# Kernel optimization log

Hardware: AMD Instinct MI355X
Metric: run time of the kernel (lower is better)

## Reference

```python
import jax, jax.numpy as jnp
import numpy as np

T, N_SAT, G_SAT, HID, IN = 256, 1024, 2048, 256, 32

def _make_sids(key):
    # per-timestep unique visible-satellite ids (matches dict-keyed state, no dup scatter)
    keys = jax.random.split(key, T)
    return jax.vmap(lambda k: jax.random.permutation(k, G_SAT)[:N_SAT])(keys).astype(jnp.int32)

def setup_inputs() -> dict:
    key = jax.random.key(0)
    ks = jax.random.split(key, 16)
    s = 0.05
    return {
        "x_rec": jax.random.normal(ks[0], (T, 1, IN), jnp.float32),
        "x_sat": jax.random.normal(ks[1], (T, N_SAT, IN), jnp.float32),
        "y_true": jax.random.normal(ks[2], (1, 2), jnp.float32),
        "W_rec": jax.random.normal(ks[3], (4, IN, HID), jnp.float32) * s,
        "b_rec": jax.random.normal(ks[4], (4, HID), jnp.float32) * s,
        "W_sat": jax.random.normal(ks[5], (4, IN, HID), jnp.float32) * s,
        "b_sat": jax.random.normal(ks[6], (4, HID), jnp.float32) * s,
        "s2r_lw": jax.random.normal(ks[7], (4, HID, HID), jnp.float32) * s,
        "s2r_lb": jax.random.normal(ks[8], (4, HID), jnp.float32) * s,
        "s2r_rw": jax.random.normal(ks[9], (4, HID, HID), jnp.float32) * s,
        "r2s_lw": jax.random.normal(ks[10], (4, HID, HID), jnp.float32) * s,
        "r2s_lb": jax.random.normal(ks[11], (4, HID), jnp.float32) * s,
        "r2s_rw": jax.random.normal(ks[12], (4, HID, HID), jnp.float32) * s,
        "W_out": jax.random.normal(ks[13], (HID, 2), jnp.float32) * s,
        "b_out": jax.random.normal(ks[14], (2,), jnp.float32) * s,
        "s_ids": _make_sids(ks[15]),
    }

def _gates(pre):
    # pre: [4, ..., HID] in gate order (i, f, c, o)
    return (jax.nn.sigmoid(pre[0]), jax.nn.sigmoid(pre[1]),
            jnp.tanh(pre[2]), jax.nn.sigmoid(pre[3]))

def reference(x_rec, x_sat, y_true, W_rec, b_rec, W_sat, b_sat,
              s2r_lw, s2r_lb, s2r_rw, r2s_lw, r2s_lb, r2s_rw,
              W_out, b_out, s_ids):
    hid = W_out.shape[0]

    def step(carry, inp):
        h_rec, c_rec, Hg, Cg = carry          # h_rec/c_rec: [hid]; Hg/Cg: [G, hid]
        xr, xs, sid = inp                      # xr: [1, in]; xs: [N, in]; sid: [N]
        h_sat = Hg[sid]                        # gather visible satellite states [N, hid]
        c_sat = Cg[sid]
        # per-gate input projections
        xr_p = jnp.einsum('i,gio->go', xr[0], W_rec) + b_rec          # [4, hid]
        xs_p = jnp.einsum('ni,gio->gno', xs, W_sat) + b_sat[:, None]  # [4, N, hid]
        # SAGEConv sat->rec: mean over all visible sats (star topology)
        mean_sat = jnp.mean(h_sat, axis=0)                            # [hid]
        conv_rec = (jnp.einsum('h,gho->go', mean_sat, s2r_lw) + s2r_lb
                    + jnp.einsum('h,gho->go', h_rec, s2r_rw))         # [4, hid]
        # SAGEConv rec->sat: each sat's sole neighbor is the receiver
        conv_sat = ((jnp.einsum('h,gho->go', h_rec, r2s_lw) + r2s_lb)[:, None, :]
                    + jnp.einsum('nh,gho->gno', h_sat, r2s_rw))       # [4, N, hid]
        i_r, f_r, t_r, o_r = _gates(xr_p + conv_rec)
        c_rec_n = f_r * c_rec + i_r * t_r
        h_rec_n = o_r * jnp.tanh(c_rec_n)
        i_s, f_s, t_s, o_s = _gates(xs_p + conv_sat)
        c_sat_n = f_s * c_sat + i_s * t_s
        h_sat_n = o_s * jnp.tanh(c_sat_n)
        Hg = Hg.at[sid].set(h_sat_n)
        Cg = Cg.at[sid].set(c_sat_n)
        return (h_rec_n, c_rec_n, Hg, Cg), None

    init = (jnp.zeros((hid,), x_rec.dtype), jnp.zeros((hid,), x_rec.dtype),
            jnp.zeros((G_SAT, hid), x_rec.dtype), jnp.zeros((G_SAT, hid), x_rec.dtype))
    (h_rec, _, _, _), _ = jax.lax.scan(step, init, (x_rec, x_sat, s_ids))
    pred = h_rec[None, :] @ W_out + b_out   # dropout is identity in eval mode
    return pred, y_true
```

## Files before the change

### kernel.cpp

```cpp
#include <hip/hip_runtime.h>
#include <cstddef>

#define T_STEPS  256
#define NSAT     1024
#define GSAT     2048
#define HID      256
#define IN_DIM   32
#define KTOT     544

typedef short  s16x8 __attribute__((ext_vector_type(8)));
typedef short  s16x4 __attribute__((ext_vector_type(4)));
typedef float  f32x4 __attribute__((ext_vector_type(4)));
typedef unsigned short ushort_t;

__device__ inline ushort_t f2bf(float f) {
    unsigned u = __builtin_bit_cast(unsigned, f);
    u += 0x7fffu + ((u >> 16) & 1u);
    return (ushort_t)(u >> 16);
}
__device__ inline float bf2f(ushort_t h) {
    unsigned u = ((unsigned)h) << 16;
    return __builtin_bit_cast(float, u);
}
__device__ inline float sigm(float x) { return 1.f / (1.f + __expf(-x)); }
__device__ inline float tanh_(float x) {
    float a = fabsf(x);
    float e = __expf(-2.f * a);
    float r = (1.f - e) / (1.f + e);
    return copysignf(r, x);
}

__global__ void k_zero(float* p, size_t n) {
    size_t i = (size_t)blockIdx.x * blockDim.x + threadIdx.x;
    size_t stride = (size_t)gridDim.x * blockDim.x;
    for (; i < n; i += stride) p[i] = 0.f;
}

__global__ void k_bconv(const float* __restrict__ r2s_rw,
                        const float* __restrict__ W_sat,
                        const float* __restrict__ r2s_lw,
                        ushort_t* __restrict__ BsatT) {
    int c = blockIdx.x;
    int g = (c >> 3) & 3, o = (c >> 5) * 8 + (c & 7);
    for (int k = threadIdx.x; k < KTOT; k += 256) {
        float v;
        if (k < 256)      v = r2s_rw[((size_t)g * 256 + k) * 256 + o];
        else if (k < 288) v = W_sat[((size_t)g * 32 + (k - 256)) * 256 + o];
        else              v = r2s_lw[((size_t)g * 256 + (k - 288)) * 256 + o];
        BsatT[(size_t)c * KTOT + k] = f2bf(v);
    }
}

__global__ void k_biasC(const float* __restrict__ r2s_lb, const float* __restrict__ b_sat,
                        float* __restrict__ biasC) {
    int c = blockIdx.x * 256 + threadIdx.x;
    if (c < 1024) {
        int g = (c >> 3) & 3, o = (c >> 5) * 8 + (c & 7);
        biasC[c] = r2s_lb[g * 256 + o] + b_sat[g * 256 + o];
    }
}

__global__ void k_inv(const int* __restrict__ s_ids, ushort_t* __restrict__ pos_inv) {
    int t = blockIdx.x;
    for (int n = threadIdx.x; n < NSAT; n += 256)
        pos_inv[(size_t)t * GSAT + s_ids[(size_t)t * NSAT + n]] = (ushort_t)(n + 1);
}

__global__ void k_asrc(const int* __restrict__ s_ids, const ushort_t* __restrict__ pos_inv,
                       int* __restrict__ asrc) {
    int t = blockIdx.x;
    for (int n = threadIdx.x; n < NSAT; n += 256) {
        int j = s_ids[(size_t)t * NSAT + n];
        int e = 1024 + j;
        if (t > 0) {
            int p = (int)pos_inv[(size_t)(t - 1) * GSAT + j] - 1;
            if (p >= 0) e = p;
        }
        asrc[(size_t)t * NSAT + n] = e;
    }
}

__global__ void k_bits(const int* __restrict__ s_ids, const ushort_t* __restrict__ pos_inv,
                       unsigned* __restrict__ nxt_bits) {
    int t = blockIdx.x, w = threadIdx.x;
    unsigned bits = 0;
    if (t + 1 < T_STEPS) {
        for (int i = 0; i < 32; i++) {
            int j = s_ids[(size_t)t * NSAT + w * 32 + i];
            if (pos_inv[(size_t)(t + 1) * GSAT + j] > 0) bits |= (1u << i);
        }
    }
    nxt_bits[t * 32 + w] = bits;
}

__global__ void k_old(const int* __restrict__ s_ids, const ushort_t* __restrict__ pos_inv,
                      short* __restrict__ old_src, int* __restrict__ old_cnt) {
    int t = blockIdx.x;
    if (t + 1 >= T_STEPS) return;
    for (int n = threadIdx.x; n < NSAT; n += 256) {
        int j = s_ids[(size_t)(t + 1) * NSAT + n];
        if (pos_inv[(size_t)t * GSAT + j] == 0) {
            int slot = atomicAdd(&old_cnt[t], 1);
            short e = (short)(-(j + 1));
            if (t > 0) {
                int p = (int)pos_inv[(size_t)(t - 1) * GSAT + j] - 1;
                if (p >= 0) e = (short)p;
            }
            old_src[(size_t)t * NSAT + slot] = e;
        }
    }
}

__global__ void k_wtb(const float* __restrict__ in, ushort_t* __restrict__ outT) {
    __shared__ float tl[32][33];
    int g = blockIdx.z;
    int h0 = blockIdx.x * 32, o0 = blockIdx.y * 32;
    int lx = threadIdx.x & 31, ly = threadIdx.x >> 5;
#pragma unroll
    for (int i = 0; i < 32; i += 8)
        tl[ly + i][lx] = in[((size_t)g * 256 + h0 + ly + i) * 256 + o0 + lx];
    __syncthreads();
#pragma unroll
    for (int i = 0; i < 32; i += 8)
        outT[((size_t)g * 256 + o0 + ly + i) * 256 + h0 + lx] = f2bf(tl[lx][ly + i]);
}

__global__ void k_wrt(const float* __restrict__ W_rec, float* __restrict__ W_recT) {
    int idx = blockIdx.x * 256 + threadIdx.x;
    int g = idx >> 8, o = idx & 255;
#pragma unroll
    for (int i = 0; i < 32; i++)
        W_recT[(size_t)idx * 32 + i] = W_rec[((size_t)g * 32 + i) * 256 + o];
}

__launch_bounds__(256)
__global__ void k_step(int t,
    const float* __restrict__ x_rec, const float* __restrict__ x_sat,
    const float* __restrict__ b_rec, const float* __restrict__ s2r_lb,
    const int* __restrict__ s_ids, const int* __restrict__ asrc,
    const unsigned* __restrict__ nxt_bits,
    const short* __restrict__ old_src, const int* __restrict__ old_cnt,
    const ushort_t* __restrict__ BsatT, const float* __restrict__ biasC,
    const ushort_t* __restrict__ s2r_rwT, const ushort_t* __restrict__ s2r_lwT,
    const float* __restrict__ W_recT,
    float* __restrict__ meanN,
    float* __restrict__ oldpart,
    float* __restrict__ crec,
    float* __restrict__ pre_rec,
    ushort_t* __restrict__ Hg_bf, float* __restrict__ Cg,
    const ushort_t* __restrict__ HnP, ushort_t* __restrict__ HnC,
    const float* __restrict__ CnP, float* __restrict__ CnC)
{
    const int b = blockIdx.x, tid = threadIdx.x;
    const float* preP  = pre_rec + ((t + 1) & 1) * 1024;
    const float* crecP = crec + (t & 1) * 256;

    if (b < 256) {
        const int by = b >> 5, bxc = b & 31;
        __shared__ ushort_t hr_bfs[256];
        __shared__ float    bias_s[32];
        __shared__ float    pre_s[128][33];

        const int w = tid >> 6, l = tid & 63;
        const int lr = l & 15, kb = (l >> 4) * 8;
        const int r0 = w * 32 + lr, r1 = r0 + 16;
        const int* asrc_t = asrc + (size_t)t * NSAT + by * 128;

        const int e0 = asrc_t[r0], e1 = asrc_t[r1];
        if (tid < 32) bias_s[tid] = biasC[bxc * 32 + tid];
        const int n_ep = tid >> 1, oi0_ep = (tid & 1) * 4;
        const int og0_ep = bxc * 8 + oi0_ep;
        const int en_ep = asrc_t[n_ep];
        const float* csrc = (en_ep < 1024) ? CnP + (size_t)en_ep * HID + og0_ep
                                           : Cg + (size_t)(en_ep - 1024) * HID + og0_ep;
        f32x4 cold = *(const f32x4*)csrc;
        ushort_t shv[4]; float scv[4]; int sjp[4];
        if (t > 0) {
#pragma unroll
            for (int i = 0; i < 4; i++) {
                int n = b * 4 + i;
                sjp[i] = s_ids[(size_t)(t - 1) * NSAT + n];
                shv[i] = HnP[(size_t)n * HID + tid];
                scv[i] = CnP[(size_t)n * HID + tid];
            }
        }
        {
            float h = 0.f;
            if (t > 0) {
                float pi = preP[tid], pf = preP[256 + tid], pc = preP[512 + tid], po = preP[768 + tid];
                float cp = (t >= 2) ? crecP[tid] : 0.f;
                float cn = sigm(pf) * cp + sigm(pi) * tanh_(pc);
                h = sigm(po) * tanh_(cn);
            }
            hr_bfs[tid] = f2bf(h);
        }

        const ushort_t* a0 = (e0 < 1024) ? HnP + (size_t)e0 * HID : Hg_bf + (size_t)(e0 - 1024) * HID;
        const ushort_t* a1 = (e1 < 1024) ? HnP + (size_t)e1 * HID : Hg_bf + (size_t)(e1 - 1024) * HID;
        const ushort_t* bp0 = BsatT + ((size_t)(bxc * 32 + lr)) * KTOT;
        const ushort_t* bp1 = bp0 + (size_t)16 * KTOT;
        f32x4 a00 = {0.f,0.f,0.f,0.f}, a01 = a00, a10 = a00, a11 = a00;
#pragma unroll
        for (int kc = 0; kc < 8; kc++) {
            int k0 = kc * 32 + kb;
            s16x8 af0 = *(const s16x8*)(a0 + k0);
            s16x8 af1 = *(const s16x8*)(a1 + k0);
            s16x8 bv0 = *(const s16x8*)(bp0 + k0);
            s16x8 bv1 = *(const s16x8*)(bp1 + k0);
            a00 = __builtin_amdgcn_mfma_f32_16x16x32_bf16(af0, bv0, a00, 0, 0, 0);
            a01 = __builtin_amdgcn_mfma_f32_16x16x32_bf16(af0, bv1, a01, 0, 0, 0);
            a10 = __builtin_amdgcn_mfma_f32_16x16x32_bf16(af1, bv0, a10, 0, 0, 0);
            a11 = __builtin_amdgcn_mfma_f32_16x16x32_bf16(af1, bv1, a11, 0, 0, 0);
        }
        {
            const float* ax0 = x_sat + ((size_t)t * NSAT + by * 128 + r0) * IN_DIM + kb;
            const float* ax1 = x_sat + ((size_t)t * NSAT + by * 128 + r1) * IN_DIM + kb;
            f32x4 x00 = *(const f32x4*)ax0, x01 = *(const f32x4*)(ax0 + 4);
            f32x4 x10 = *(const f32x4*)ax1, x11 = *(const f32x4*)(ax1 + 4);
            s16x8 af0, af1;
#pragma unroll
            for (int e = 0; e < 4; e++) {
                af0[e] = (short)f2bf(x00[e]); af0[4 + e] = (short)f2bf(x01[e]);
                af1[e] = (short)f2bf(x10[e]); af1[4 + e] = (short)f2bf(x11[e]);
            }
            int k0 = 256 + kb;
            s16x8 bv0 = *(const s16x8*)(bp0 + k0);
            s16x8 bv1 = *(const s16x8*)(bp1 + k0);
            a00 = __builtin_amdgcn_mfma_f32_16x16x32_bf16(af0, bv0, a00, 0, 0, 0);
            a01 = __builtin_amdgcn_mfma_f32_16x16x32_bf16(af0, bv1, a01, 0, 0, 0);
            a10 = __builtin_amdgcn_mfma_f32_16x16x32_bf16(af1, bv0, a10, 0, 0, 0);
            a11 = __builtin_amdgcn_mfma_f32_16x16x32_bf16(af1, bv1, a11, 0, 0, 0);
        }
        __syncthreads();
#pragma unroll
        for (int kc = 0; kc < 8; kc++) {
            int k0 = 288 + kc * 32 + kb;
            s16x8 af = *(const s16x8*)(hr_bfs + (k0 - 288));
            s16x8 bv0 = *(const s16x8*)(bp0 + k0);
            s16x8 bv1 = *(const s16x8*)(bp1 + k0);
            a00 = __builtin_amdgcn_mfma_f32_16x16x32_bf16(af, bv0, a00, 0, 0, 0);
            a01 = __builtin_amdgcn_mfma_f32_16x16x32_bf16(af, bv1, a01, 0, 0, 0);
            a10 = __builtin_amdgcn_mfma_f32_16x16x32_bf16(af, bv0, a10, 0, 0, 0);
            a11 = __builtin_amdgcn_mfma_f32_16x16x32_bf16(af, bv1, a11, 0, 0, 0);
        }
#pragma unroll
        for (int rr = 0; rr < 4; rr++) {
            int ro = (l >> 4) * 4 + rr;
            pre_s[w * 32 + ro][lr]           = a00[rr];
            pre_s[w * 32 + ro][16 + lr]      = a01[rr];
            pre_s[w * 32 + 16 + ro][lr]      = a10[rr];
            pre_s[w * 32 + 16 + ro][16 + lr] = a11[rr];
        }
        __syncthreads();

        {
            int n = n_ep, oi0 = oi0_ep, og0 = og0_ep;
            int gr = by * 128 + n;
            bool nxt = (t + 1 < T_STEPS) && ((nxt_bits[t * 32 + (gr >> 5)] >> (gr & 31)) & 1u);
            f32x4 cnew, hf; s16x4 hnew;
#pragma unroll
            for (int e = 0; e < 4; e++) {
                int oi = oi0 + e;
                float pi = pre_s[n][oi]      + bias_s[oi];
                float pf = pre_s[n][8 + oi]  + bias_s[8 + oi];
                float pc = pre_s[n][16 + oi] + bias_s[16 + oi];
                float po = pre_s[n][24 + oi] + bias_s[24 + oi];
                float ig = sigm(pi), fg = sigm(pf), tg = tanh_(pc), oo = sigm(po);
                float cn = fg * cold[e] + ig * tg;
                float hn = oo * tanh_(cn);
                cnew[e] = cn; hf[e] = hn;
                hnew[e] = (short)f2bf(hn);
            }
            *(f32x4*)(CnC + (size_t)gr * HID + og0) = cnew;
            *(s16x4*)(HnC + (size_t)gr * HID + og0) = hnew;
#pragma unroll
            for (int e = 0; e < 4; e++) pre_s[n][oi0 + e] = nxt ? hf[e] : 0.f;
        }
        __syncthreads();
        if (t + 1 < T_STEPS && tid < 8) {
            float s = 0.f;
            for (int n = 0; n < 128; n++) s += pre_s[n][tid];
            meanN[((t + 1) & 1) * 2048 + by * 256 + bxc * 8 + tid] = s;
        }

        if (t > 0) {
#pragma unroll
            for (int i = 0; i < 4; i++) {
                Hg_bf[(size_t)sjp[i] * HID + tid] = shv[i];
                Cg[(size_t)sjp[i] * HID + tid]    = scv[i];
            }
        }
    } else {
        const int r = b - 256;
        __shared__ float mean_s[256], hr_s[256], xr_s[32];
        const int m_old = (t + 1 < T_STEPS) ? old_cnt[t] : 0;
        {
            float s = 0.f;
            const float* mp = meanN + (t & 1) * 2048;
#pragma unroll
            for (int p = 0; p < 8; p++) s += mp[p * 256 + tid];
            const float* op = oldpart + (t & 1) * 8192;
#pragma unroll 8
            for (int p = 0; p < 32; p++) s += op[p * 256 + tid];
            mean_s[tid] = s * (1.f / 1024.f);
        }
        {
            float h = 0.f, cn = 0.f;
            if (t > 0) {
                float pi = preP[tid], pf = preP[256 + tid], pc = preP[512 + tid], po = preP[768 + tid];
                float cp = (t >= 2) ? crecP[tid] : 0.f;
                cn = sigm(pf) * cp + sigm(pi) * tanh_(pc);
                h = sigm(po) * tanh_(cn);
            }
            hr_s[tid] = h;
            if (r == 0 && t > 0) crec[((t + 1) & 1) * 256 + tid] = cn;
        }
        if (tid < 32) xr_s[tid] = x_rec[(size_t)t * IN_DIM + tid];
        __syncthreads();
        float s_old = 0.f;
        {
            const short* osp = old_src + (size_t)t * NSAT;
#pragma unroll 2
            for (int k = r; k < m_old; k += 32) {
                int e = osp[k];
                const ushort_t* hp = (e >= 0) ? HnP + (size_t)e * HID
                                              : Hg_bf + (size_t)(-(e + 1)) * HID;
                s_old += bf2f(hp[tid]);
            }
        }
        {
            const int combo = tid >> 3, sub = tid & 7;
            const int g = combo >> 3, oo = combo & 7;
            const int o = r * 8 + oo;
            const ushort_t* rwp = s2r_rwT + ((size_t)(g * 256 + o)) * 256 + sub * 32;
            const ushort_t* lwp = s2r_lwT + ((size_t)(g * 256 + o)) * 256 + sub * 32;
            float part = 0.f;
#pragma unroll
            for (int q = 0; q < 4; q++) {
                s16x8 a = *(const s16x8*)(rwp + q * 8);
                s16x8 c = *(const s16x8*)(lwp + q * 8);
#pragma unroll
                for (int e = 0; e < 8; e++) {
                    int h = sub * 32 + q * 8 + e;
                    part += hr_s[h] * bf2f((ushort_t)a[e]) + mean_s[h] * bf2f((ushort_t)c[e]);
                }
            }
            {
                f32x4 wx = *(const f32x4*)(W_recT + ((size_t)(g * 256 + o)) * 32 + sub * 4);
#pragma unroll
                for (int e = 0; e < 4; e++) part += xr_s[sub * 4 + e] * wx[e];
            }
            part += __shfl_down(part, 4);
            part += __shfl_down(part, 2);
            part += __shfl_down(part, 1);
            if (sub == 0)
                pre_rec[(t & 1) * 1024 + g * 256 + o] =
                    part + b_rec[g * HID + o] + s2r_lb[g * HID + o];
        }
        if (t + 1 < T_STEPS)
            oldpart[((t + 1) & 1) * 8192 + r * 256 + tid] = s_old;
    }
}

__global__ void k_final(const float* __restrict__ pre_rec,
                        const float* __restrict__ crec,
                        const float* __restrict__ W_out,
                        const float* __restrict__ b_out,
                        const float* __restrict__ y_true,
                        float* __restrict__ out) {
    __shared__ float red[256];
    int o = threadIdx.x;
    const float* pre = pre_rec + ((T_STEPS - 1) & 1) * 1024;
    float pi = pre[o], pf = pre[256 + o], pc = pre[512 + o], po = pre[768 + o];
    float cp = crec[(T_STEPS & 1) * 256 + o];
    float cn = sigm(pf) * cp + sigm(pi) * tanh_(pc);
    float h = sigm(po) * tanh_(cn);
    for (int j = 0; j < 2; j++) {
        red[o] = h * W_out[o * 2 + j];
        __syncthreads();
        for (int s = 128; s > 0; s >>= 1) {
            if (o < s) red[o] += red[o + s];
            __syncthreads();
        }
        if (o == 0) out[j] = red[0] + b_out[j];
        __syncthreads();
    }
    if (o < 2) out[2 + o] = y_true[o];
}

extern "C" void kernel_launch(void* const* d_in, const int* in_sizes, int n_in,
                              void* d_out, int out_size, void* d_ws, size_t ws_size,
                              hipStream_t stream) {
    (void)in_sizes; (void)n_in; (void)out_size; (void)ws_size;
    const float* x_rec  = (const float*)d_in[0];
    const float* x_sat  = (const float*)d_in[1];
    const float* y_true = (const float*)d_in[2];
    const float* W_rec  = (const float*)d_in[3];
    const float* b_rec  = (const float*)d_in[4];
    const float* W_sat  = (const float*)d_in[5];
    const float* b_sat  = (const float*)d_in[6];
    const float* s2r_lw = (const float*)d_in[7];
    const float* s2r_lb = (const float*)d_in[8];
    const float* s2r_rw = (const float*)d_in[9];
    const float* r2s_lw = (const float*)d_in[10];
    const float* r2s_lb = (const float*)d_in[11];
    const float* r2s_rw = (const float*)d_in[12];
    const float* W_out  = (const float*)d_in[13];
    const float* b_out  = (const float*)d_in[14];
    const int*   s_ids  = (const int*)d_in[15];

    float* ws = (float*)d_ws;
    size_t off = 0;
    float*    meanN    = ws + off;              off += 4096;
    float*    oldpart  = ws + off;              off += 16384;
    float*    crec     = ws + off;              off += 512;
    float*    pre_rec  = ws + off;              off += 2048;
    int*      old_cnt  = (int*)(ws + off);      off += 256;
    ushort_t* Hg_bf    = (ushort_t*)(ws + off); off += 262144;
    float*    Cg       = ws + off;              off += 524288;
    ushort_t* pos_inv  = (ushort_t*)(ws + off); off += 262144;
    int*      asrc     = (int*)(ws + off);      off += 262144;
    unsigned* nxt_bits = (unsigned*)(ws + off); off += 8192;
    short*    old_src  = (short*)(ws + off);    off += 131072;
    ushort_t* HnewA    = (ushort_t*)(ws + off); off += 131072;
    ushort_t* HnewB    = (ushort_t*)(ws + off); off += 131072;
    float*    CnewA    = ws + off;              off += 262144;
    float*    CnewB    = ws + off;              off += 262144;
    ushort_t* BsatT    = (ushort_t*)(ws + off); off += 278528;
    float*    biasC    = ws + off;              off += 1024;
    ushort_t* s2r_rwT  = (ushort_t*)(ws + off); off += 131072;
    ushort_t* s2r_lwT  = (ushort_t*)(ws + off); off += 131072;
    float*    W_recT   = ws + off;              off += 32768;

    const size_t zcount = 4096 + 16384 + 512 + 2048 + 256 + 262144 + 524288 + 262144;
    hipLaunchKernelGGL(k_zero, dim3(2048), dim3(256), 0, stream, ws, zcount);
    hipLaunchKernelGGL(k_inv, dim3(T_STEPS), dim3(256), 0, stream, s_ids, pos_inv);
    hipLaunchKernelGGL(k_asrc, dim3(T_STEPS), dim3(256), 0, stream, s_ids, pos_inv, asrc);
    hipLaunchKernelGGL(k_bits, dim3(T_STEPS), dim3(32), 0, stream, s_ids, pos_inv, nxt_bits);
    hipLaunchKernelGGL(k_old, dim3(T_STEPS), dim3(256), 0, stream, s_ids, pos_inv, old_src, old_cnt);
    hipLaunchKernelGGL(k_bconv, dim3(1024), dim3(256), 0, stream, r2s_rw, W_sat, r2s_lw, BsatT);
    hipLaunchKernelGGL(k_biasC, dim3(4), dim3(256), 0, stream, r2s_lb, b_sat, biasC);
    hipLaunchKernelGGL(k_wtb, dim3(8, 8, 4), dim3(256), 0, stream, s2r_rw, s2r_rwT);
    hipLaunchKernelGGL(k_wtb, dim3(8, 8, 4), dim3(256), 0, stream, s2r_lw, s2r_lwT);
    hipLaunchKernelGGL(k_wrt, dim3(4), dim3(256), 0, stream, W_rec, W_recT);

    for (int t = 0; t < T_STEPS; t++) {
        const ushort_t* HnP = (t & 1) ? HnewA : HnewB;
        ushort_t*       HnC = (t & 1) ? HnewB : HnewA;
        const float*    CnP = (t & 1) ? CnewA : CnewB;
        float*          CnC = (t & 1) ? CnewB : CnewA;
        hipLaunchKernelGGL(k_step, dim3(288), dim3(256), 0, stream,
                           t, x_rec, x_sat, b_rec, s2r_lb,
                           s_ids, asrc, nxt_bits, old_src, old_cnt,
                           BsatT, biasC,
                           s2r_rwT, s2r_lwT, W_recT,
                           meanN, oldpart, crec, pre_rec,
                           Hg_bf, Cg, HnP, HnC, CnP, CnC);
    }
    hipLaunchKernelGGL(k_final, dim3(1), dim3(256), 0, stream,
                       pre_rec, crec, W_out, b_out, y_true, (float*)d_out);
}
```

Before: 3.604 ms.

## Hoist receiver r2s term out of MFMA, store cell state in bf16, write back only leavers

The receiver-to-satellite left-weight product is the same for every satellite row, so it is taken out of the per-row MFMA K loop (K shrinks from 544 to 288). Each block now computes it once as a small dot product into shared memory and adds it like a bias. Satellite cell state (global and ping-pong buffers) moves from fp32 to bf16, halving its traffic. Writebacks to the global state now cover only satellites that leave visibility, using a precomputed leaver list, instead of all previous-step rows. Storing the cell state in bf16 adds rounding error that builds up along the recurrence.

```diff
diff --git a/kernel.cpp b/kernel.cpp
--- a/kernel.cpp
+++ b/kernel.cpp
@@ -6,7 +6,7 @@
 #define GSAT     2048
 #define HID      256
 #define IN_DIM   32
-#define KTOT     544
+#define KTOT     288
 
 typedef short  s16x8 __attribute__((ext_vector_type(8)));
 typedef short  s16x4 __attribute__((ext_vector_type(4)));
@@ -38,17 +38,21 @@
 
 __global__ void k_bconv(const float* __restrict__ r2s_rw,
                         const float* __restrict__ W_sat,
-                        const float* __restrict__ r2s_lw,
                         ushort_t* __restrict__ BsatT) {
     int c = blockIdx.x;
     int g = (c >> 3) & 3, o = (c >> 5) * 8 + (c & 7);
     for (int k = threadIdx.x; k < KTOT; k += 256) {
-        float v;
-        if (k < 256)      v = r2s_rw[((size_t)g * 256 + k) * 256 + o];
-        else if (k < 288) v = W_sat[((size_t)g * 32 + (k - 256)) * 256 + o];
-        else              v = r2s_lw[((size_t)g * 256 + (k - 288)) * 256 + o];
+        float v = (k < 256) ? r2s_rw[((size_t)g * 256 + k) * 256 + o]
+                            : W_sat[((size_t)g * 32 + (k - 256)) * 256 + o];
         BsatT[(size_t)c * KTOT + k] = f2bf(v);
     }
+}
+
+__global__ void k_rlw(const float* __restrict__ r2s_lw, ushort_t* __restrict__ rlw_bf) {
+    int c = blockIdx.x;
+    int g = (c >> 3) & 3, o = (c >> 5) * 8 + (c & 7);
+    int h = threadIdx.x;
+    rlw_bf[(size_t)c * 256 + h] = f2bf(r2s_lw[((size_t)g * 256 + h) * 256 + o]);
 }
 
 __global__ void k_biasC(const float* __restrict__ r2s_lb, const float* __restrict__ b_sat,
@@ -111,6 +115,19 @@
     }
 }
 
+__global__ void k_lv(const int* __restrict__ s_ids, const ushort_t* __restrict__ pos_inv,
+                     int* __restrict__ lv, int* __restrict__ lv_cnt) {
+    int t = blockIdx.x;
+    if (t == 0) return;
+    for (int n = threadIdx.x; n < NSAT; n += 256) {
+        int j = s_ids[(size_t)(t - 1) * NSAT + n];
+        if (pos_inv[(size_t)t * GSAT + j] == 0) {
+            int slot = atomicAdd(&lv_cnt[t], 1);
+            lv[(size_t)t * NSAT + slot] = (n << 16) | j;
+        }
+    }
+}
+
 __global__ void k_wtb(const float* __restrict__ in, ushort_t* __restrict__ outT) {
     __shared__ float tl[32][33];
     int g = blockIdx.z;
@@ -137,19 +154,20 @@
 __global__ void k_step(int t,
     const float* __restrict__ x_rec, const float* __restrict__ x_sat,
     const float* __restrict__ b_rec, const float* __restrict__ s2r_lb,
-    const int* __restrict__ s_ids, const int* __restrict__ asrc,
-    const unsigned* __restrict__ nxt_bits,
+    const int* __restrict__ asrc, const unsigned* __restrict__ nxt_bits,
     const short* __restrict__ old_src, const int* __restrict__ old_cnt,
-    const ushort_t* __restrict__ BsatT, const float* __restrict__ biasC,
+    const int* __restrict__ lv, const int* __restrict__ lv_cnt,
+    const ushort_t* __restrict__ BsatT, const ushort_t* __restrict__ rlw_bf,
+    const float* __restrict__ biasC,
     const ushort_t* __restrict__ s2r_rwT, const ushort_t* __restrict__ s2r_lwT,
     const float* __restrict__ W_recT,
     float* __restrict__ meanN,
     float* __restrict__ oldpart,
     float* __restrict__ crec,
     float* __restrict__ pre_rec,
-    ushort_t* __restrict__ Hg_bf, float* __restrict__ Cg,
+    ushort_t* __restrict__ Hg_bf, ushort_t* __restrict__ Cg_bf,
     const ushort_t* __restrict__ HnP, ushort_t* __restrict__ HnC,
-    const float* __restrict__ CnP, float* __restrict__ CnC)
+    const ushort_t* __restrict__ CnP, ushort_t* __restrict__ CnC)
 {
     const int b = blockIdx.x, tid = threadIdx.x;
     const float* preP  = pre_rec + ((t + 1) & 1) * 1024;
@@ -159,6 +177,7 @@
         const int by = b >> 5, bxc = b & 31;
         __shared__ ushort_t hr_bfs[256];
         __shared__ float    bias_s[32];
+        __shared__ float    rl_s[32];
         __shared__ float    pre_s[128][33];
 
         const int w = tid >> 6, l = tid & 63;
@@ -171,18 +190,20 @@
         const int n_ep = tid >> 1, oi0_ep = (tid & 1) * 4;
         const int og0_ep = bxc * 8 + oi0_ep;
         const int en_ep = asrc_t[n_ep];
-        const float* csrc = (en_ep < 1024) ? CnP + (size_t)en_ep * HID + og0_ep
-                                           : Cg + (size_t)(en_ep - 1024) * HID + og0_ep;
-        f32x4 cold = *(const f32x4*)csrc;
-        ushort_t shv[4]; float scv[4]; int sjp[4];
-        if (t > 0) {
-#pragma unroll
-            for (int i = 0; i < 4; i++) {
-                int n = b * 4 + i;
-                sjp[i] = s_ids[(size_t)(t - 1) * NSAT + n];
-                shv[i] = HnP[(size_t)n * HID + tid];
-                scv[i] = CnP[(size_t)n * HID + tid];
-            }
+        const ushort_t* csrc = (en_ep < 1024) ? CnP + (size_t)en_ep * HID + og0_ep
+                                              : Cg_bf + (size_t)(en_ep - 1024) * HID + og0_ep;
+        s16x4 cold4 = *(const s16x4*)csrc;
+        const int lv_m = lv_cnt[t];
+        ushort_t pH[4], pC[4]; int pJ[4];
+#pragma unroll
+        for (int i = 0; i < 4; i++) {
+            int k = b + i * 256;
+            if (k < lv_m) {
+                int pv = lv[(size_t)t * NSAT + k];
+                int pos = pv >> 16; pJ[i] = pv & 0xffff;
+                pH[i] = HnP[(size_t)pos * HID + tid];
+                pC[i] = CnP[(size_t)pos * HID + tid];
+            } else pJ[i] = -1;
         }
         {
             float h = 0.f;
@@ -231,18 +252,6 @@
             a10 = __builtin_amdgcn_mfma_f32_16x16x32_bf16(af1, bv0, a10, 0, 0, 0);
             a11 = __builtin_amdgcn_mfma_f32_16x16x32_bf16(af1, bv1, a11, 0, 0, 0);
         }
-        __syncthreads();
-#pragma unroll
-        for (int kc = 0; kc < 8; kc++) {
-            int k0 = 288 + kc * 32 + kb;
-            s16x8 af = *(const s16x8*)(hr_bfs + (k0 - 288));
-            s16x8 bv0 = *(const s16x8*)(bp0 + k0);
-            s16x8 bv1 = *(const s16x8*)(bp1 + k0);
-            a00 = __builtin_amdgcn_mfma_f32_16x16x32_bf16(af, bv0, a00, 0, 0, 0);
-            a01 = __builtin_amdgcn_mfma_f32_16x16x32_bf16(af, bv1, a01, 0, 0, 0);
-            a10 = __builtin_amdgcn_mfma_f32_16x16x32_bf16(af, bv0, a10, 0, 0, 0);
-            a11 = __builtin_amdgcn_mfma_f32_16x16x32_bf16(af, bv1, a11, 0, 0, 0);
-        }
 #pragma unroll
         for (int rr = 0; rr < 4; rr++) {
             int ro = (l >> 4) * 4 + rr;
@@ -254,24 +263,43 @@
         __syncthreads();
 
         {
+            int c = tid >> 3, sub = tid & 7;
+            const ushort_t* wp = rlw_bf + ((size_t)(bxc * 32 + c)) * 256 + sub * 32;
+            float acc = 0.f;
+#pragma unroll
+            for (int q = 0; q < 4; q++) {
+                s16x8 wv = *(const s16x8*)(wp + q * 8);
+#pragma unroll
+                for (int e = 0; e < 8; e++)
+                    acc += bf2f(hr_bfs[sub * 32 + q * 8 + e]) * bf2f((ushort_t)wv[e]);
+            }
+            acc += __shfl_down(acc, 4);
+            acc += __shfl_down(acc, 2);
+            acc += __shfl_down(acc, 1);
+            if (sub == 0) rl_s[c] = acc + bias_s[c];
+        }
+        __syncthreads();
+
+        {
             int n = n_ep, oi0 = oi0_ep, og0 = og0_ep;
             int gr = by * 128 + n;
             bool nxt = (t + 1 < T_STEPS) && ((nxt_bits[t * 32 + (gr >> 5)] >> (gr & 31)) & 1u);
-            f32x4 cnew, hf; s16x4 hnew;
+            f32x4 hf; s16x4 cnew, hnew;
 #pragma unroll
             for (int e = 0; e < 4; e++) {
                 int oi = oi0 + e;
-                float pi = pre_s[n][oi]      + bias_s[oi];
-                float pf = pre_s[n][8 + oi]  + bias_s[8 + oi];
-                float pc = pre_s[n][16 + oi] + bias_s[16 + oi];
-                float po = pre_s[n][24 + oi] + bias_s[24 + oi];
+                float pi = pre_s[n][oi]      + rl_s[oi];
+                float pf = pre_s[n][8 + oi]  + rl_s[8 + oi];
+                float pc = pre_s[n][16 + oi] + rl_s[16 + oi];
+                float po = pre_s[n][24 + oi] + rl_s[24 + oi];
                 float ig = sigm(pi), fg = sigm(pf), tg = tanh_(pc), oo = sigm(po);
-                float cn = fg * cold[e] + ig * tg;
+                float cn = fg * bf2f((ushort_t)cold4[e]) + ig * tg;
                 float hn = oo * tanh_(cn);
-                cnew[e] = cn; hf[e] = hn;
+                hf[e] = hn;
+                cnew[e] = (short)f2bf(cn);
                 hnew[e] = (short)f2bf(hn);
             }
-            *(f32x4*)(CnC + (size_t)gr * HID + og0) = cnew;
+            *(s16x4*)(CnC + (size_t)gr * HID + og0) = cnew;
             *(s16x4*)(HnC + (size_t)gr * HID + og0) = hnew;
 #pragma unroll
             for (int e = 0; e < 4; e++) pre_s[n][oi0 + e] = nxt ? hf[e] : 0.f;
@@ -283,11 +311,11 @@
             meanN[((t + 1) & 1) * 2048 + by * 256 + bxc * 8 + tid] = s;
         }
 
-        if (t > 0) {
-#pragma unroll
-            for (int i = 0; i < 4; i++) {
-                Hg_bf[(size_t)sjp[i] * HID + tid] = shv[i];
-                Cg[(size_t)sjp[i] * HID + tid]    = scv[i];
+#pragma unroll
+        for (int i = 0; i < 4; i++) {
+            if (pJ[i] >= 0) {
+                Hg_bf[(size_t)pJ[i] * HID + tid] = pH[i];
+                Cg_bf[(size_t)pJ[i] * HID + tid] = pC[i];
             }
         }
     } else {
@@ -416,29 +444,35 @@
     float*    crec     = ws + off;              off += 512;
     float*    pre_rec  = ws + off;              off += 2048;
     int*      old_cnt  = (int*)(ws + off);      off += 256;
+    int*      lv_cnt   = (int*)(ws + off);      off += 256;
     ushort_t* Hg_bf    = (ushort_t*)(ws + off); off += 262144;
-    float*    Cg       = ws + off;              off += 524288;
+    ushort_t* Cg_bf    = (ushort_t*)(ws + off); off += 262144;
     ushort_t* pos_inv  = (ushort_t*)(ws + off); off += 262144;
     int*      asrc     = (int*)(ws + off);      off += 262144;
     unsigned* nxt_bits = (unsigned*)(ws + off); off += 8192;
     short*    old_src  = (short*)(ws + off);    off += 131072;
+    int*      lv       = (int*)(ws + off);      off += 262144;
     ushort_t* HnewA    = (ushort_t*)(ws + off); off += 131072;
     ushort_t* HnewB    = (ushort_t*)(ws + off); off += 131072;
-    float*    CnewA    = ws + off;              off += 262144;
-    float*    CnewB    = ws + off;              off += 262144;
-    ushort_t* BsatT    = (ushort_t*)(ws + off); off += 278528;
+    ushort_t* CnewA    = (ushort_t*)(ws + off); off += 131072;
+    ushort_t* CnewB    = (ushort_t*)(ws + off); off += 131072;
+    ushort_t* BsatT    = (ushort_t*)(ws + off); off += 147456;
+    ushort_t* rlw_bf   = (ushort_t*)(ws + off); off += 131072;
     float*    biasC    = ws + off;              off += 1024;
     ushort_t* s2r_rwT  = (ushort_t*)(ws + off); off += 131072;
     ushort_t* s2r_lwT  = (ushort_t*)(ws + off); off += 131072;
     float*    W_recT   = ws + off;              off += 32768;
 
-    const size_t zcount = 4096 + 16384 + 512 + 2048 + 256 + 262144 + 524288 + 262144;
+    const size_t zcount = 4096 + 16384 + 512 + 2048 + 256 + 256
+                        + 262144 + 262144 + 262144;
     hipLaunchKernelGGL(k_zero, dim3(2048), dim3(256), 0, stream, ws, zcount);
     hipLaunchKernelGGL(k_inv, dim3(T_STEPS), dim3(256), 0, stream, s_ids, pos_inv);
     hipLaunchKernelGGL(k_asrc, dim3(T_STEPS), dim3(256), 0, stream, s_ids, pos_inv, asrc);
     hipLaunchKernelGGL(k_bits, dim3(T_STEPS), dim3(32), 0, stream, s_ids, pos_inv, nxt_bits);
     hipLaunchKernelGGL(k_old, dim3(T_STEPS), dim3(256), 0, stream, s_ids, pos_inv, old_src, old_cnt);
-    hipLaunchKernelGGL(k_bconv, dim3(1024), dim3(256), 0, stream, r2s_rw, W_sat, r2s_lw, BsatT);
+    hipLaunchKernelGGL(k_lv, dim3(T_STEPS), dim3(256), 0, stream, s_ids, pos_inv, lv, lv_cnt);
+    hipLaunchKernelGGL(k_bconv, dim3(1024), dim3(256), 0, stream, r2s_rw, W_sat, BsatT);
+    hipLaunchKernelGGL(k_rlw, dim3(1024), dim3(256), 0, stream, r2s_lw, rlw_bf);
     hipLaunchKernelGGL(k_biasC, dim3(4), dim3(256), 0, stream, r2s_lb, b_sat, biasC);
     hipLaunchKernelGGL(k_wtb, dim3(8, 8, 4), dim3(256), 0, stream, s2r_rw, s2r_rwT);
     hipLaunchKernelGGL(k_wtb, dim3(8, 8, 4), dim3(256), 0, stream, s2r_lw, s2r_lwT);
@@ -447,15 +481,15 @@
     for (int t = 0; t < T_STEPS; t++) {
         const ushort_t* HnP = (t & 1) ? HnewA : HnewB;
         ushort_t*       HnC = (t & 1) ? HnewB : HnewA;
-        const float*    CnP = (t & 1) ? CnewA : CnewB;
-        float*          CnC = (t & 1) ? CnewB : CnewA;
+        const ushort_t* CnP = (t & 1) ? CnewA : CnewB;
+        ushort_t*       CnC = (t & 1) ? CnewB : CnewA;
         hipLaunchKernelGGL(k_step, dim3(288), dim3(256), 0, stream,
                            t, x_rec, x_sat, b_rec, s2r_lb,
-                           s_ids, asrc, nxt_bits, old_src, old_cnt,
-                           BsatT, biasC,
+                           asrc, nxt_bits, old_src, old_cnt, lv, lv_cnt,
+                           BsatT, rlw_bf, biasC,
                            s2r_rwT, s2r_lwT, W_recT,
                            meanN, oldpart, crec, pre_rec,
-                           Hg_bf, Cg, HnP, HnC, CnP, CnC);
+                           Hg_bf, Cg_bf, HnP, HnC, CnP, CnC);
     }
     hipLaunchKernelGGL(k_final, dim3(1), dim3(256), 0, stream,
                        pre_rec, crec, W_out, b_out, y_true, (float*)d_out);
```

Result: faster. 3.378 ms (-6.3%).
